# Performance work log

Hardware: AMD Instinct MI355X
Metric: run time of the kernel (lower is better)

Reference implementation:

```python
import jax, jax.numpy as jnp
import numpy as np

HIDDEN = 1152
PATCH = 16
POS_SIZE = 64
B = 16
NP_ = 4096
IN_DIM = 3 * PATCH * PATCH  # 768


def setup_inputs() -> dict:
    key = jax.random.key(0)
    k1, k2, k3, k4, k5 = jax.random.split(key, 5)
    pixel_values = jax.random.normal(k1, (B, NP_, IN_DIM), dtype=jnp.float32)
    pixel_position_ids = jax.random.randint(k2, (B, NP_, 2), 0, POS_SIZE, dtype=jnp.int64)
    padding_positions = jax.random.randint(k3, (B, NP_), 0, 2) > 0
    # learned params: nn.Linear(input_dim, hidden, bias=False) weight is [hidden, in_dim]
    W = jax.random.normal(k4, (HIDDEN, IN_DIM), dtype=jnp.float32) / np.sqrt(IN_DIM)
    table = jax.random.normal(k5, (2, POS_SIZE, HIDDEN), dtype=jnp.float32)
    return {
        "pixel_values": pixel_values,
        "pixel_position_ids": pixel_position_ids,
        "padding_positions": padding_positions,
        "W": W,
        "table": table,
    }


def reference(pixel_values, pixel_position_ids, padding_positions, W, table):
    # input_proj: [B, N, in_dim] @ W.T -> [B, N, hidden]
    hidden_states = jnp.einsum("bnd,hd->bnh", pixel_values, W)
    # one_hot + matmul + sum over axis-of-2 is exactly a gather of the x-row
    # from table[0] plus the y-row from table[1]
    pos = jnp.clip(pixel_position_ids, 0, None)  # [B, N, 2]
    pe = table[0][pos[..., 0]] + table[1][pos[..., 1]]  # [B, N, hidden]
    pe = jnp.where(padding_positions[..., None], jnp.zeros_like(pe), pe)
    return hidden_states + pe
```

## Files before the change

kernel.cpp:

```cpp
#include <hip/hip_runtime.h>

#define HIDDEN 1152
#define IN_DIM 768
#define POS_SIZE 64
#define M_TOTAL (16 * 4096)

#define BM 64
#define LDA 776
#define NPASS 6
#define NSTAGE 12
#define TOTSTAGE (NPASS * NSTAGE)

typedef _Float16 f16x8 __attribute__((ext_vector_type(8)));
typedef float f32x4 __attribute__((ext_vector_type(4)));
typedef float f32x8v __attribute__((ext_vector_type(8)));

typedef __attribute__((address_space(1))) const void global_cv;
typedef __attribute__((address_space(3))) void lds_v;

__device__ __forceinline__ void async16(const void* g, void* l) {
    __builtin_amdgcn_global_load_lds((global_cv*)g, (lds_v*)l, 16, 0, 0);
}

__global__ __launch_bounds__(256) void pack_w(const float* __restrict__ W,
                                              _Float16* __restrict__ Wp) {
    unsigned tid = blockIdx.x * 256 + threadIdx.x;
    unsigned n = tid / 96u;
    unsigned kc = tid - n * 96u;
    f32x8v x = *(const f32x8v*)(W + (size_t)n * IN_DIM + kc * 8u);
    f16x8 h = __builtin_convertvector(x, f16x8);
    unsigned c = (n >> 4) * 1536u + kc * 16u + (n & 15u);
    ((f16x8*)Wp)[c] = h;
}

__device__ __forceinline__ void stageB(const f16x8* wp, _Float16* dstBuf,
                                       int t, int pass, int s) {
#pragma unroll
    for (int i = 0; i < 3; i++) {
        int c = t + i * 512;
        int kk = c / 768;
        int rem = c - kk * 768;
        int n16l = rem >> 6;
        int lc = rem & 63;
        size_t srcIdx = (size_t)(pass * 12 + n16l) * 1536 +
                        (size_t)(2 * s + kk) * 64 + lc;
        async16(wp + srcIdx, dstBuf + (size_t)c * 8);
    }
}

__global__ __launch_bounds__(512, 2) void gemm_pe(
    const float* __restrict__ A,
    const _Float16* __restrict__ Wp,
    const int* __restrict__ pos,
    const int* __restrict__ pad,
    const float* __restrict__ table,
    float* __restrict__ out) {
    __shared__ __align__(16) _Float16 sA[BM * LDA];
    __shared__ __align__(16) _Float16 sB[2][12288];

    const int m0 = blockIdx.x * BM;
    const int t = threadIdx.x;
    const int lane = t & 63;
    const int w = t >> 6;
    const int quad = lane >> 4;
    const int l15 = lane & 15;
    const int mw = w >> 2;
    const int nw = w & 3;
    const int arow0 = mw * 32 + l15;

    const f16x8* wp = (const f16x8*)Wp;

    stageB(wp, sB[0], t, 0, 0);

    int pxv[8], pyv[8], pdv[8];
#pragma unroll
    for (int mi = 0; mi < 2; mi++)
#pragma unroll
        for (int r = 0; r < 4; r++) {
            const int gm = m0 + mw * 32 + mi * 16 + quad * 4 + r;
            int px = pos[gm * 2];
            int py = pos[gm * 2 + 1];
            pxv[mi * 4 + r] = px < 0 ? 0 : px;
            pyv[mi * 4 + r] = py < 0 ? 0 : py;
            pdv[mi * 4 + r] = pad[gm];
        }

    {
        const float* gA = A + (size_t)m0 * IN_DIM;
#pragma unroll 4
        for (int i = 0; i < 12; i++) {
            int c = t + i * 512;
            int row = c / 96;
            int col8 = c - row * 96;
            f32x8v x = *(const f32x8v*)(gA + (size_t)row * IN_DIM + col8 * 8);
            f16x8 h = __builtin_convertvector(x, f16x8);
            *(f16x8*)&sA[row * LDA + col8 * 8] = h;
        }
    }
    __syncthreads();

    for (int pass = 0; pass < NPASS; pass++) {
        f32x4 acc[2][3];
#pragma unroll
        for (int mi = 0; mi < 2; mi++)
#pragma unroll
            for (int ni = 0; ni < 3; ni++) acc[mi][ni] = (f32x4)0.f;

        for (int s = 0; s < NSTAGE; s++) {
            const int g = pass * NSTAGE + s;
            if (g < TOTSTAGE - 1) {
                const int gn = g + 1;
                const int pn = gn / NSTAGE;
                const int sn = gn - pn * NSTAGE;
                stageB(wp, sB[gn & 1], t, pn, sn);
                asm volatile("s_waitcnt vmcnt(3)" ::: "memory");
            } else {
                asm volatile("s_waitcnt vmcnt(0)" ::: "memory");
            }
            asm volatile("s_barrier" ::: "memory");

            const _Float16* bbuf = sB[g & 1];
            f16x8 af[2][2], bf[3][2];
#pragma unroll
            for (int mi = 0; mi < 2; mi++)
#pragma unroll
                for (int kk = 0; kk < 2; kk++)
                    af[mi][kk] = *(const f16x8*)&sA[(arow0 + mi * 16) * LDA +
                                                    (2 * s + kk) * 32 + quad * 8];
#pragma unroll
            for (int ni = 0; ni < 3; ni++)
#pragma unroll
                for (int kk = 0; kk < 2; kk++)
                    bf[ni][kk] = *(const f16x8*)&bbuf[((kk * 12 + nw * 3 + ni) * 64 +
                                                       lane) * 8];
#pragma unroll
            for (int kk = 0; kk < 2; kk++)
#pragma unroll
                for (int mi = 0; mi < 2; mi++)
#pragma unroll
                    for (int ni = 0; ni < 3; ni++)
                        acc[mi][ni] = __builtin_amdgcn_mfma_f32_16x16x32_f16(
                            af[mi][kk], bf[ni][kk], acc[mi][ni], 0, 0, 0);
            asm volatile("s_barrier" ::: "memory");
        }

        const int gn0 = pass * 192 + nw * 48;
#pragma unroll
        for (int mi = 0; mi < 2; mi++) {
#pragma unroll
            for (int r = 0; r < 4; r++) {
                const int gm = m0 + mw * 32 + mi * 16 + quad * 4 + r;
                const int idx = mi * 4 + r;
                const float* rx = table + (size_t)pxv[idx] * HIDDEN;
                const float* ry = table + (size_t)(POS_SIZE + pyv[idx]) * HIDDEN;
                float* orow = out + (size_t)gm * HIDDEN;
                const int isPad = pdv[idx];
#pragma unroll
                for (int ni = 0; ni < 3; ni++) {
                    const int gn = gn0 + ni * 16 + l15;
                    float pe = isPad ? 0.f : (rx[gn] + ry[gn]);
                    orow[gn] = acc[mi][ni][r] + pe;
                }
            }
        }
    }
}

__global__ __launch_bounds__(256) void fallback_naive(const float* __restrict__ A,
                                                      const float* __restrict__ W,
                                                      const int* __restrict__ pos,
                                                      const int* __restrict__ pad,
                                                      const float* __restrict__ table,
                                                      float* __restrict__ out) {
    long idx = (long)blockIdx.x * 256 + threadIdx.x;
    const long total = (long)M_TOTAL * HIDDEN;
    if (idx >= total) return;
    int m = (int)(idx / HIDDEN);
    int n = (int)(idx - (long)m * HIDDEN);
    const float* a = A + (size_t)m * IN_DIM;
    const float* wv = W + (size_t)n * IN_DIM;
    float s = 0.f;
    for (int k = 0; k < IN_DIM; k++) s += a[k] * wv[k];
    int px = pos[m * 2]; if (px < 0) px = 0;
    int py = pos[m * 2 + 1]; if (py < 0) py = 0;
    float pe = pad[m] ? 0.f : (table[(size_t)px * HIDDEN + n] +
                               table[(size_t)(POS_SIZE + py) * HIDDEN + n]);
    out[idx] = s + pe;
}

extern "C" void kernel_launch(void* const* d_in, const int* in_sizes, int n_in,
                              void* d_out, int out_size, void* d_ws, size_t ws_size,
                              hipStream_t stream) {
    const float* pixel = (const float*)d_in[0];
    const int* pos = (const int*)d_in[1];
    const int* pad = (const int*)d_in[2];
    const float* W = (const float*)d_in[3];
    const float* table = (const float*)d_in[4];
    float* out = (float*)d_out;

    const size_t nW = (size_t)HIDDEN * IN_DIM;
    if (ws_size >= nW * sizeof(_Float16)) {
        _Float16* Wp = (_Float16*)d_ws;
        pack_w<<<432, 256, 0, stream>>>(W, Wp);
        gemm_pe<<<M_TOTAL / BM, 512, 0, stream>>>(pixel, Wp, pos, pad, table, out);
    } else {
        long total = (long)M_TOTAL * HIDDEN;
        fallback_naive<<<(int)((total + 255) / 256), 256, 0, stream>>>(pixel, W, pos, pad,
                                                                       table, out);
    }
}
```

Baseline: 648.7 us.

## Triple-buffer W stages, shrink per-pass N tile, swizzle A in LDS

Each pass now covers 128 columns of N instead of 192, so there are nine passes, and the W stage buffer grows from two slots to three with a prefetch distance of two. The A tile in LDS goes from a padded row layout to a k-chunk-major layout with an XOR row swizzle, which shrinks LDS use and is meant to avoid bank conflicts. s_setprio is raised around the MFMA block. Together these aim to hide global-to-LDS latency better and lower LDS pressure, at the cost of more passes and barriers and less MFMA work per barrier.

```diff
diff --git a/kernel.cpp b/kernel.cpp
--- a/kernel.cpp
+++ b/kernel.cpp
@@ -6,8 +6,7 @@
 #define M_TOTAL (16 * 4096)
 
 #define BM 64
-#define LDA 776
-#define NPASS 6
+#define NPASS 9
 #define NSTAGE 12
 #define TOTSTAGE (NPASS * NSTAGE)
 
@@ -34,16 +33,16 @@
 }
 
 __device__ __forceinline__ void stageB(const f16x8* wp, _Float16* dstBuf,
-                                       int t, int pass, int s) {
-#pragma unroll
-    for (int i = 0; i < 3; i++) {
+                                       int t, int g) {
+    int p = g / NSTAGE;
+    int s = g - p * NSTAGE;
+#pragma unroll
+    for (int i = 0; i < 2; i++) {
         int c = t + i * 512;
-        int kk = c / 768;
-        int rem = c - kk * 768;
-        int n16l = rem >> 6;
-        int lc = rem & 63;
-        size_t srcIdx = (size_t)(pass * 12 + n16l) * 1536 +
-                        (size_t)(2 * s + kk) * 64 + lc;
+        int kk = c >> 9;
+        int n16l = (c >> 6) & 7;
+        int lc = c & 63;
+        size_t srcIdx = (size_t)(p * 8 + n16l) * 1536 + (size_t)(2 * s + kk) * 64 + lc;
         async16(wp + srcIdx, dstBuf + (size_t)c * 8);
     }
 }
@@ -55,8 +54,8 @@
     const int* __restrict__ pad,
     const float* __restrict__ table,
     float* __restrict__ out) {
-    __shared__ __align__(16) _Float16 sA[BM * LDA];
-    __shared__ __align__(16) _Float16 sB[2][12288];
+    __shared__ __align__(16) _Float16 sA[6144 * 8];
+    __shared__ __align__(16) _Float16 sB[3][8192];
 
     const int m0 = blockIdx.x * BM;
     const int t = threadIdx.x;
@@ -66,11 +65,11 @@
     const int l15 = lane & 15;
     const int mw = w >> 2;
     const int nw = w & 3;
-    const int arow0 = mw * 32 + l15;
 
     const f16x8* wp = (const f16x8*)Wp;
 
-    stageB(wp, sB[0], t, 0, 0);
+    stageB(wp, sB[0], t, 0);
+    stageB(wp, sB[1], t, 1);
 
     int pxv[8], pyv[8], pdv[8];
 #pragma unroll
@@ -91,60 +90,68 @@
         for (int i = 0; i < 12; i++) {
             int c = t + i * 512;
             int row = c / 96;
-            int col8 = c - row * 96;
-            f32x8v x = *(const f32x8v*)(gA + (size_t)row * IN_DIM + col8 * 8);
+            int kc = c - row * 96;
+            f32x8v x = *(const f32x8v*)(gA + (size_t)row * IN_DIM + kc * 8);
             f16x8 h = __builtin_convertvector(x, f16x8);
-            *(f16x8*)&sA[row * LDA + col8 * 8] = h;
+            int chunk = kc * 64 + (row ^ ((kc & 7) << 1));
+            *(f16x8*)&sA[(size_t)chunk * 8] = h;
         }
     }
     __syncthreads();
 
+    const int arow_base = mw * 32 + l15;
+
     for (int pass = 0; pass < NPASS; pass++) {
-        f32x4 acc[2][3];
+        f32x4 acc[2][2];
 #pragma unroll
         for (int mi = 0; mi < 2; mi++)
 #pragma unroll
-            for (int ni = 0; ni < 3; ni++) acc[mi][ni] = (f32x4)0.f;
+            for (int ni = 0; ni < 2; ni++) acc[mi][ni] = (f32x4)0.f;
 
         for (int s = 0; s < NSTAGE; s++) {
             const int g = pass * NSTAGE + s;
-            if (g < TOTSTAGE - 1) {
-                const int gn = g + 1;
-                const int pn = gn / NSTAGE;
-                const int sn = gn - pn * NSTAGE;
-                stageB(wp, sB[gn & 1], t, pn, sn);
-                asm volatile("s_waitcnt vmcnt(3)" ::: "memory");
+            if (g < TOTSTAGE - 2) {
+                const int g2 = g + 2;
+                stageB(wp, sB[g2 - (g2 / 3) * 3], t, g2);
+                asm volatile("s_waitcnt vmcnt(4)" ::: "memory");
+            } else if (g == TOTSTAGE - 2) {
+                asm volatile("s_waitcnt vmcnt(2)" ::: "memory");
             } else {
                 asm volatile("s_waitcnt vmcnt(0)" ::: "memory");
             }
             asm volatile("s_barrier" ::: "memory");
 
-            const _Float16* bbuf = sB[g & 1];
-            f16x8 af[2][2], bf[3][2];
+            const _Float16* bbuf = sB[g - (g / 3) * 3];
+            f16x8 af[2][2], bf[2][2];
 #pragma unroll
             for (int mi = 0; mi < 2; mi++)
 #pragma unroll
+                for (int kk = 0; kk < 2; kk++) {
+                    const int kc = (2 * s + kk) * 4 + quad;
+                    const int row = (arow_base + mi * 16) ^ ((kc & 7) << 1);
+                    af[mi][kk] = *(const f16x8*)&sA[(size_t)(kc * 64 + row) * 8];
+                }
+#pragma unroll
+            for (int ni = 0; ni < 2; ni++)
+#pragma unroll
                 for (int kk = 0; kk < 2; kk++)
-                    af[mi][kk] = *(const f16x8*)&sA[(arow0 + mi * 16) * LDA +
-                                                    (2 * s + kk) * 32 + quad * 8];
-#pragma unroll
-            for (int ni = 0; ni < 3; ni++)
-#pragma unroll
-                for (int kk = 0; kk < 2; kk++)
-                    bf[ni][kk] = *(const f16x8*)&bbuf[((kk * 12 + nw * 3 + ni) * 64 +
-                                                       lane) * 8];
+                    bf[ni][kk] = *(const f16x8*)&bbuf[(size_t)((kk * 8 + nw * 2 + ni) * 64 +
+                                                               lane) * 8];
+
+            __builtin_amdgcn_s_setprio(1);
 #pragma unroll
             for (int kk = 0; kk < 2; kk++)
 #pragma unroll
                 for (int mi = 0; mi < 2; mi++)
 #pragma unroll
-                    for (int ni = 0; ni < 3; ni++)
+                    for (int ni = 0; ni < 2; ni++)
                         acc[mi][ni] = __builtin_amdgcn_mfma_f32_16x16x32_f16(
                             af[mi][kk], bf[ni][kk], acc[mi][ni], 0, 0, 0);
+            __builtin_amdgcn_s_setprio(0);
             asm volatile("s_barrier" ::: "memory");
         }
 
-        const int gn0 = pass * 192 + nw * 48;
+        const int gn0 = pass * 128 + nw * 32;
 #pragma unroll
         for (int mi = 0; mi < 2; mi++) {
 #pragma unroll
@@ -156,7 +163,7 @@
                 float* orow = out + (size_t)gm * HIDDEN;
                 const int isPad = pdv[idx];
 #pragma unroll
-                for (int ni = 0; ni < 3; ni++) {
+                for (int ni = 0; ni < 2; ni++) {
                     const int gn = gn0 + ni * 16 + l15;
                     float pe = isPad ? 0.f : (rx[gn] + ry[gn]);
                     orow[gn] = acc[mi][ni][r] + pe;
```

After: 616.4 us. 5.0% less time.
